# Performance work log

Measured on AMD Instinct MI355X. Metric: run time of the kernel, lower is better.

The kernel has to match this reference:

```python
import jax, jax.numpy as jnp
import numpy as np

B, S, D = 8, 2048, 64
H = 128


def setup_inputs() -> dict:
    key = jax.random.key(0)
    k = jax.random.split(key, 5)
    X = jax.random.normal(k[0], (B, S, D), dtype=jnp.float32)
    Wi = jax.random.normal(k[1], (H, D), dtype=jnp.float32)          # init_layer weight, std=1
    bi = jax.random.normal(k[2], (H,), dtype=jnp.float32)            # init_layer bias, std=1
    Wa = jax.random.normal(k[3], (H * H, D + 1), dtype=jnp.float32) / jnp.sqrt(H)  # vf_A, std=1/sqrt(H)
    Wb = jax.random.normal(k[4], (H, D + 1), dtype=jnp.float32)      # vf_B, std=1
    return {"X": X, "Wi": Wi, "bi": bi, "Wa": Wa, "Wb": Wb}


def reference(X, Wi, bi, Wa, Wb):
    b, s, d = X.shape
    dt = 1.0 / (s - 1)
    # inp: time channel (constant dt) concatenated with scaled input -> [b, s, d+1]
    inp = jnp.concatenate([jnp.full((b, s, 1), dt, dtype=X.dtype), X * dt], axis=-1)
    y0 = X[:, 0] @ Wi.T + bi                       # [b, H]
    Bs = jnp.einsum('bsk,hk->bsh', inp[:, 1:], Wb)  # [b, s-1, H]

    def step(y, xs):
        inp_t, b_t = xs                            # [b, d+1], [b, H]
        A = (inp_t @ Wa.T).reshape(b, H, H)        # per-step transition matrix
        y_new = y + jnp.einsum('bij,bj->bi', A, y) + b_t
        return y_new, y_new

    xs = (jnp.swapaxes(inp[:, 1:], 0, 1), jnp.swapaxes(Bs, 0, 1))  # time-major
    _, ys_rest = jax.lax.scan(step, y0, xs)        # [s-1, b, H]
    ys = jnp.concatenate([y0[:, None, :], jnp.swapaxes(ys_rest, 0, 1)], axis=1)
    return ys
```

## Files before the change

### kernel.cpp

```cpp
#include <hip/hip_runtime.h>
#include <hip/hip_fp16.h>
#include <hip/hip_cooperative_groups.h>

namespace cg = cooperative_groups;


typedef _Float16 h8 __attribute__((ext_vector_type(8)));
typedef float v4f __attribute__((ext_vector_type(4)));
typedef unsigned int uint;

constexpr int B_ = 8, S_ = 2048, D_ = 64, H_ = 128;
constexpr int T_ = S_ - 1;
constexpr int KD = D_ + 1;
constexpr float DTC = 1.0f / 2047.0f;
constexpr int L_ = 8;
constexpr int LSH = 3;
constexpr int NC = 256;

__global__ __launch_bounds__(256) void k_prep(const float* __restrict__ Wa,
                                              _Float16* __restrict__ Wa16B,
                                              float* __restrict__ Wa0,
                                              const float* __restrict__ X,
                                              _Float16* __restrict__ Xs16,
                                              const float* __restrict__ Wb,
                                              float* __restrict__ Bs,
                                              const float* __restrict__ Wi,
                                              const float* __restrict__ bi,
                                              float* __restrict__ out,
                                              float* __restrict__ yb) {
  __shared__ float wb_s[H_ * KD];
  __shared__ float xs[16][D_ + 4];
  int bx = blockIdx.x, tid = threadIdx.x;
  if (bx < 4096) {
    int idx = bx * 256 + tid;
    int r = idx >> 6, kk = idx & 63;
    int rt = r >> 4, n = r & 15;
    int kb = kk >> 5, q = (kk >> 3) & 3, jj = kk & 7;
    float v = Wa[(size_t)r * KD + 1 + kk];
    Wa16B[((((size_t)rt * 2 + kb) * 4 + q) * 16 + n) * 8 + jj] = (_Float16)v;
    if (kk == 0) Wa0[r] = Wa[(size_t)r * KD];
  } else if (bx < 8190) {
    int idx = (bx - 4096) * 256 + tid;
    if (idx < B_ * T_ * 64) {
      int bt = idx >> 6, d = idx & 63;
      int b = bt / T_, s = bt - b * T_;
      Xs16[(size_t)bt * 64 + d] = (_Float16)(X[((size_t)b * S_ + s + 1) * D_ + d] * DTC);
    }
  } else if (bx < 9214) {
    int bt0 = (bx - 8190) * 16;
    for (int i2 = tid; i2 < H_ * KD; i2 += 256) wb_s[i2] = Wb[i2];
    for (int i2 = tid; i2 < 16 * D_; i2 += 256) {
      int sl = i2 >> 6, d = i2 & 63;
      int btg = bt0 + sl;
      float v = 0.f;
      if (btg < B_ * T_) {
        int b = btg / T_, s = btg - b * T_;
        v = X[((size_t)b * S_ + s + 1) * D_ + d] * DTC;
      }
      xs[sl][d] = v;
    }
    __syncthreads();
    int h = tid & 127, sh = tid >> 7;
    const float* wrow = &wb_s[h * KD];
    for (int u = 0; u < 8; u++) {
      int sl = sh * 8 + u;
      int btg = bt0 + sl;
      if (btg >= B_ * T_) break;
      float acc = wrow[0] * DTC;
#pragma unroll 8
      for (int d = 0; d < D_; d++) acc += xs[sl][d] * wrow[1 + d];
      Bs[(size_t)btg * H_ + h] = acc;
    }
  } else {
    int b = bx - 9214;
    if (tid < D_) xs[0][tid] = X[(size_t)b * S_ * D_ + tid];
    __syncthreads();
    if (tid < H_) {
      float acc = bi[tid];
      const float* wr = Wi + tid * D_;
#pragma unroll 8
      for (int d = 0; d < D_; d++) acc += xs[0][d] * wr[d];
      out[(size_t)b * S_ * H_ + tid] = acc;
      yb[(size_t)(b * NC + 0) * H_ + tid] = acc;
    }
  }
}

__global__ __launch_bounds__(256) void k_amat(const _Float16* __restrict__ Xs16,
                                              const _Float16* __restrict__ Wa16B,
                                              const float* __restrict__ Wa0,
                                              _Float16* __restrict__ A_sl,
                                              int c0, int scShift) {
  __shared__ _Float16 sb[32 * 528];
  int tid = threadIdx.x;
  int w = tid >> 6, lane = tid & 63;
  int n = lane & 15, q = lane >> 4;
  int rowbase = blockIdx.x * 32;
  int SCm = ((1 << scShift) << LSH) - 1;

  h8 af[2][2];
#pragma unroll
  for (int mi = 0; mi < 2; mi++) {
    int sidx = rowbase + mi * 16 + n;
    int b = sidx >> (scShift + LSH);
    int rem = sidx & SCm;
    int cc = rem >> LSH, l = rem & (L_ - 1);
    int s = (c0 + cc) * L_ + l;
    if (s >= T_) s = T_ - 1;
    size_t btg = (size_t)b * T_ + s;
#pragma unroll
    for (int kb = 0; kb < 2; kb++)
      af[mi][kb] = *(const h8*)(Xs16 + btg * 64 + kb * 32 + q * 8);
  }

  v4f acc[2][8];
#pragma unroll
  for (int nj = 0; nj < 8; nj++) {
    int ct_g = blockIdx.y * 32 + w * 8 + nj;
    float binit = DTC * Wa0[ct_g * 16 + n];
    h8 bf0 = *(const h8*)(Wa16B + ((((size_t)ct_g * 2 + 0) * 4 + q) * 16 + n) * 8);
    h8 bf1 = *(const h8*)(Wa16B + ((((size_t)ct_g * 2 + 1) * 4 + q) * 16 + n) * 8);
#pragma unroll
    for (int mi = 0; mi < 2; mi++) {
      v4f a;
      a[0] = binit; a[1] = binit; a[2] = binit; a[3] = binit;
      a = __builtin_amdgcn_mfma_f32_16x16x32_f16(af[mi][0], bf0, a, 0, 0, 0);
      a = __builtin_amdgcn_mfma_f32_16x16x32_f16(af[mi][1], bf1, a, 0, 0, 0);
      acc[mi][nj] = a;
    }
  }
#pragma unroll
  for (int mi = 0; mi < 2; mi++)
#pragma unroll
    for (int nj = 0; nj < 8; nj++)
#pragma unroll
      for (int reg = 0; reg < 4; reg++)
        sb[(mi * 16 + q * 4 + reg) * 528 + w * 128 + ((nj * 16 + n) ^ (q * 16))] =
            (_Float16)acc[mi][nj][reg];
  __syncthreads();
#pragma unroll
  for (int it = 0; it < 8; it++) {
    int idx = tid + it * 256;
    int t = idx >> 6, u4 = idx & 63;
    int qt = (t >> 2) & 3;
    uint4 val = *(const uint4*)&sb[t * 528 + ((u4 * 8) ^ (qt * 16))];
    *(uint4*)(A_sl + (size_t)(rowbase + t) * 16384 + blockIdx.y * 512 + u4 * 8) = val;
  }
}

__device__ __forceinline__ void chunkmap_body(const _Float16* __restrict__ A_sl,
                                              const float* __restrict__ Bs,
                                              _Float16* __restrict__ Mr,
                                              float* __restrict__ vch,
                                              int c0, int scShift, int chunk, int tid,
                                              _Float16* Dt, float* v32) {
  int w = tid >> 6, lane = tid & 63;
  int n = lane & 15, q = lane >> 4;
  int SC = 1 << scShift;
  int b = chunk >> scShift;
  int cc = chunk & (SC - 1);
  int c = c0 + cc;
  int sbase = c * L_;
  int nsteps = min(L_, T_ - sbase);
  const _Float16* Abase = A_sl + (size_t)chunk * L_ * 16384;
  size_t btb = (size_t)b * T_ + sbase;

#pragma unroll
  for (int it = 0; it < 8; it++) {
    int idx = tid + it * 256;
    int rowl = idx & 127, c8 = (idx >> 7) * 8;
    uint4 pk = *(const uint4*)(Abase + rowl * 128 + c8);
    const _Float16* hp = (const _Float16*)&pk;
#pragma unroll
    for (int cx = 0; cx < 8; cx++) Dt[(c8 + cx) * 136 + rowl] = hp[cx];
  }
  if (tid < 128) v32[tid] = Bs[btb * 128 + tid];
  h8 idE, idO;
#pragma unroll
  for (int jj = 0; jj < 8; jj++) {
    idE[jj] = (_Float16)((q * 8 + jj == n) ? 1.f : 0.f);
    idO[jj] = (_Float16)((q * 8 + jj == 16 + n) ? 1.f : 0.f);
  }
  __syncthreads();

  v4f acc[2][8];
#pragma unroll
  for (int mi = 0; mi < 2; mi++) {
    int row0 = (2 * w + mi) * 16 + q * 4;
#pragma unroll
    for (int nj = 0; nj < 8; nj++) {
      int col = nj * 16 + n;
      union { uint2 u; _Float16 h[4]; } m2;
      m2.u = *(const uint2*)&Dt[col * 136 + row0];
#pragma unroll
      for (int reg = 0; reg < 4; reg++) acc[mi][nj][reg] = (float)m2.h[reg];
    }
  }

  int r0 = 2 * w * 16 + n, r1 = r0 + 16;
  h8 afA[2][4], afB[2][4];

#define LOADA(dst, l)                                                                \
  {                                                                                  \
    const _Float16* Ag = Abase + (size_t)(l) * 16384;                                \
    _Pragma("unroll")                                                                \
    for (int mi = 0; mi < 2; mi++)                                                   \
      _Pragma("unroll")                                                              \
      for (int kb = 0; kb < 4; kb++)                                                 \
        dst[mi][kb] = *(const h8*)(Ag + ((2 * w + mi) * 16 + n) * 128 + kb * 32 + q * 8); \
  }

#define STEPQ(af, l)                                                                 \
  {                                                                                  \
    _Pragma("unroll")                                                                \
    for (int nj = 0; nj < 8; nj++) {                                                 \
      h8 bfr[4];                                                                     \
      _Pragma("unroll")                                                              \
      for (int kb = 0; kb < 4; kb++)                                                 \
        bfr[kb] = *(const h8*)&Dt[(nj * 16 + n) * 136 + kb * 32 + q * 8];            \
      _Pragma("unroll")                                                              \
      for (int mi = 0; mi < 2; mi++) {                                               \
        _Pragma("unroll")                                                            \
        for (int kb = 0; kb < 4; kb++)                                               \
          acc[mi][nj] = __builtin_amdgcn_mfma_f32_16x16x32_f16(af[mi][kb], bfr[kb], acc[mi][nj], 0, 0, 0); \
        acc[mi][nj] = __builtin_amdgcn_mfma_f32_16x16x32_f16(                        \
            af[mi][nj >> 1], (nj & 1) ? idO : idE, acc[mi][nj], 0, 0, 0);            \
      }                                                                              \
    }                                                                                \
    float dv0 = 0.f, dv1 = 0.f;                                                      \
    _Pragma("unroll")                                                                \
    for (int kb = 0; kb < 4; kb++) {                                                 \
      float4 p0 = *(const float4*)&v32[kb * 32 + q * 8];                             \
      float4 p1 = *(const float4*)&v32[kb * 32 + q * 8 + 4];                         \
      float vk[8] = {p0.x, p0.y, p0.z, p0.w, p1.x, p1.y, p1.z, p1.w};                \
      _Pragma("unroll")                                                              \
      for (int jj = 0; jj < 8; jj++) {                                               \
        dv0 += (float)af[0][kb][jj] * vk[jj];                                        \
        dv1 += (float)af[1][kb][jj] * vk[jj];                                        \
      }                                                                              \
    }                                                                                \
    dv0 += __shfl_xor(dv0, 16); dv0 += __shfl_xor(dv0, 32);                          \
    dv1 += __shfl_xor(dv1, 16); dv1 += __shfl_xor(dv1, 32);                          \
    float vold0 = v32[r0], vold1 = v32[r1];                                          \
    float bs0 = 0.f, bs1 = 0.f;                                                      \
    if (q == 0) {                                                                    \
      bs0 = Bs[(btb + (l)) * 128 + r0];                                              \
      bs1 = Bs[(btb + (l)) * 128 + r1];                                              \
    }                                                                                \
    __syncthreads();                                                                 \
    _Pragma("unroll")                                                                \
    for (int mi = 0; mi < 2; mi++) {                                                 \
      int row0 = (2 * w + mi) * 16 + q * 4;                                          \
      _Pragma("unroll")                                                              \
      for (int nj = 0; nj < 8; nj++) {                                               \
        int col = nj * 16 + n;                                                       \
        union { _Float16 h[4]; uint2 u; } pk;                                        \
        _Pragma("unroll")                                                            \
        for (int reg = 0; reg < 4; reg++) pk.h[reg] = (_Float16)acc[mi][nj][reg];    \
        *(uint2*)&Dt[col * 136 + row0] = pk.u;                                       \
      }                                                                              \
    }                                                                                \
    if (q == 0) {                                                                    \
      v32[r0] = vold0 + dv0 + bs0;                                                   \
      v32[r1] = vold1 + dv1 + bs1;                                                   \
    }                                                                                \
    __syncthreads();                                                                 \
  }

  LOADA(afA, 1);
  for (int l = 1; l < nsteps; l += 2) {
    if (l + 1 < nsteps) LOADA(afB, l + 1);
    STEPQ(afA, l);
    if (l + 2 < nsteps) LOADA(afA, l + 2);
    if (l + 1 < nsteps) STEPQ(afB, l + 1);
  }
#undef LOADA
#undef STEPQ

#pragma unroll
  for (int mi = 0; mi < 2; mi++) {
    int row0 = (2 * w + mi) * 16 + q * 4;
#pragma unroll
    for (int nj = 0; nj < 8; nj++) {
      int col = nj * 16 + n;
#pragma unroll
      for (int reg = 0; reg < 4; reg++)
        Dt[(row0 + reg) * 136 + col] = (_Float16)acc[mi][nj][reg];
    }
  }
  __syncthreads();
  _Float16* og = Mr + (size_t)chunk * 16384;
#pragma unroll
  for (int it = 0; it < 8; it++) {
    int idx = tid + it * 256;
    int rowl = idx >> 4, ch = idx & 15;
    uint4 val = *(const uint4*)&Dt[rowl * 136 + ch * 8];
    *(uint4*)(og + rowl * 128 + ch * 8) = val;
  }
  if (tid < 128) vch[(size_t)chunk * 128 + tid] = v32[tid];
}

__device__ __forceinline__ void comp4_body(const _Float16* __restrict__ in_map,
                                           const float* __restrict__ in_v,
                                           _Float16* __restrict__ out_map,
                                           float* __restrict__ out_v,
                                           int outIdx, int tid,
                                           _Float16* Dt, float* v32) {
  int w = tid >> 6, lane = tid & 63;
  int n = lane & 15, q = lane >> 4;
  size_t nbase = (size_t)outIdx * 4;

  const _Float16* P0 = in_map + nbase * 16384;
#pragma unroll
  for (int it = 0; it < 8; it++) {
    int idx = tid + it * 256;
    int rowl = idx & 127, c8 = (idx >> 7) * 8;
    uint4 pk = *(const uint4*)(P0 + rowl * 128 + c8);
    const _Float16* hp = (const _Float16*)&pk;
#pragma unroll
    for (int cx = 0; cx < 8; cx++) Dt[(c8 + cx) * 136 + rowl] = hp[cx];
  }
  if (tid < 128) v32[tid] = in_v[nbase * 128 + tid];
  h8 idE, idO;
#pragma unroll
  for (int jj = 0; jj < 8; jj++) {
    idE[jj] = (_Float16)((q * 8 + jj == n) ? 1.f : 0.f);
    idO[jj] = (_Float16)((q * 8 + jj == 16 + n) ? 1.f : 0.f);
  }
  __syncthreads();

  v4f acc[2][8];
#pragma unroll
  for (int mi = 0; mi < 2; mi++) {
    int row0 = (2 * w + mi) * 16 + q * 4;
#pragma unroll
    for (int nj = 0; nj < 8; nj++) {
      int col = nj * 16 + n;
      union { uint2 u; _Float16 h[4]; } m2;
      m2.u = *(const uint2*)&Dt[col * 136 + row0];
#pragma unroll
      for (int reg = 0; reg < 4; reg++) acc[mi][nj][reg] = (float)m2.h[reg];
    }
  }

  int r0 = 2 * w * 16 + n, r1 = r0 + 16;
  for (int j = 1; j < 4; j++) {
    const _Float16* Pj = in_map + (nbase + j) * 16384;
    h8 af[2][4];
#pragma unroll
    for (int mi = 0; mi < 2; mi++)
#pragma unroll
      for (int kb = 0; kb < 4; kb++)
        af[mi][kb] = *(const h8*)(Pj + ((2 * w + mi) * 16 + n) * 128 + kb * 32 + q * 8);
#pragma unroll
    for (int nj = 0; nj < 8; nj++) {
      h8 bfr[4];
#pragma unroll
      for (int kb = 0; kb < 4; kb++)
        bfr[kb] = *(const h8*)&Dt[(nj * 16 + n) * 136 + kb * 32 + q * 8];
#pragma unroll
      for (int mi = 0; mi < 2; mi++) {
#pragma unroll
        for (int kb = 0; kb < 4; kb++)
          acc[mi][nj] = __builtin_amdgcn_mfma_f32_16x16x32_f16(af[mi][kb], bfr[kb], acc[mi][nj], 0, 0, 0);
        acc[mi][nj] = __builtin_amdgcn_mfma_f32_16x16x32_f16(
            af[mi][nj >> 1], (nj & 1) ? idO : idE, acc[mi][nj], 0, 0, 0);
      }
    }
    float dv0 = 0.f, dv1 = 0.f;
#pragma unroll
    for (int kb = 0; kb < 4; kb++) {
      float4 p0 = *(const float4*)&v32[kb * 32 + q * 8];
      float4 p1 = *(const float4*)&v32[kb * 32 + q * 8 + 4];
      float vk[8] = {p0.x, p0.y, p0.z, p0.w, p1.x, p1.y, p1.z, p1.w};
#pragma unroll
      for (int jj = 0; jj < 8; jj++) {
        dv0 += (float)af[0][kb][jj] * vk[jj];
        dv1 += (float)af[1][kb][jj] * vk[jj];
      }
    }
    dv0 += __shfl_xor(dv0, 16); dv0 += __shfl_xor(dv0, 32);
    dv1 += __shfl_xor(dv1, 16); dv1 += __shfl_xor(dv1, 32);
    float vold0 = v32[r0], vold1 = v32[r1];
    float vj0 = 0.f, vj1 = 0.f;
    if (q == 0) {
      vj0 = in_v[(nbase + j) * 128 + r0];
      vj1 = in_v[(nbase + j) * 128 + r1];
    }
    __syncthreads();
#pragma unroll
    for (int mi = 0; mi < 2; mi++) {
      int row0 = (2 * w + mi) * 16 + q * 4;
#pragma unroll
      for (int nj = 0; nj < 8; nj++) {
        int col = nj * 16 + n;
        union { _Float16 h[4]; uint2 u; } pk;
#pragma unroll
        for (int reg = 0; reg < 4; reg++) pk.h[reg] = (_Float16)acc[mi][nj][reg];
        *(uint2*)&Dt[col * 136 + row0] = pk.u;
      }
    }
    if (q == 0) {
      v32[r0] = vold0 + dv0 + vj0;
      v32[r1] = vold1 + dv1 + vj1;
    }
    __syncthreads();
  }
#pragma unroll
  for (int mi = 0; mi < 2; mi++) {
    int row0 = (2 * w + mi) * 16 + q * 4;
#pragma unroll
    for (int nj = 0; nj < 8; nj++) {
      int col = nj * 16 + n;
#pragma unroll
      for (int reg = 0; reg < 4; reg++)
        Dt[(row0 + reg) * 136 + col] = (_Float16)acc[mi][nj][reg];
    }
  }
  __syncthreads();
  _Float16* og = out_map + (size_t)outIdx * 16384;
#pragma unroll
  for (int it = 0; it < 8; it++) {
    int idx = tid + it * 256;
    int rowl = idx >> 4, ch = idx & 15;
    uint4 val = *(const uint4*)&Dt[rowl * 136 + ch * 8];
    *(uint4*)(og + rowl * 128 + ch * 8) = val;
  }
  if (tid < 128) out_v[(size_t)outIdx * 128 + tid] = v32[tid];
}

__device__ __forceinline__ void chainsuper_body(const _Float16* __restrict__ Sr,
                                                const float* __restrict__ sv,
                                                float* __restrict__ yb,
                                                int c0, int scShift, int b, int tid,
                                                float* ybuf, float* red) {
  int NS = 1 << (scShift - 2);
  int i = tid >> 1, hh = tid & 1;
  if (tid < 128) ybuf[tid] = yb[(size_t)(b * NC + c0) * 128 + tid];
  __syncthreads();

  uint4 arA[8], arB[8];
  float svA, svB;

#define LOADS(ar, svv, s)                                                            \
  {                                                                                  \
    const uint4* p = (const uint4*)(Sr + (size_t)(b * NS + (s)) * 16384 + i * 128 + hh * 64); \
    _Pragma("unroll")                                                                \
    for (int u = 0; u < 8; u++) ar[u] = p[u];                                        \
    svv = sv[(size_t)(b * NS + (s)) * 128 + i];                                      \
  }

#define STEPS(ar, svv, s)                                                            \
  {                                                                                  \
    float pt = 0.f;                                                                  \
    _Pragma("unroll")                                                                \
    for (int u = 0; u < 8; u++) {                                                    \
      union { uint4 v; _Float16 h[8]; } wv; wv.v = ar[u];                            \
      _Pragma("unroll")                                                              \
      for (int k = 0; k < 8; k++) pt += (float)wv.h[k] * ybuf[hh * 64 + u * 8 + k];  \
    }                                                                                \
    if (hh) red[i] = pt;                                                             \
    __syncthreads();                                                                 \
    if (!hh) {                                                                       \
      float yn = ybuf[i] + pt + red[i] + svv;                                        \
      int cg = c0 + 4 * ((s) + 1);                                                   \
      if (cg < NC) yb[(size_t)(b * NC + cg) * 128 + i] = yn;                         \
      ybuf[i] = yn;                                                                  \
    }                                                                                \
    __syncthreads();                                                                 \
  }

  LOADS(arA, svA, 0);
  int s = 0;
  for (; s + 1 < NS; s += 2) {
    LOADS(arB, svB, s + 1);
    STEPS(arA, svA, s);
    if (s + 2 < NS) LOADS(arA, svA, s + 2);
    STEPS(arB, svB, s + 1);
  }
  if (s < NS) STEPS(arA, svA, s);
#undef LOADS
#undef STEPS
}

__device__ __forceinline__ void emit_body(const _Float16* __restrict__ A_sl,
                                          const float* __restrict__ Bs,
                                          const _Float16* __restrict__ Mr,
                                          const float* __restrict__ vch,
                                          const float* __restrict__ yb,
                                          float* __restrict__ out,
                                          int tid, int b, int c, int kpre, int cbase,
                                          int nst, size_t node0, size_t sidx0, size_t btb,
                                          uint4* arA, float bsA, uint4* arP, float vvP,
                                          float* ybuf, float* red) {
  int i = tid >> 1, hh = tid & 1;
  if (tid < 128) ybuf[tid] = yb[(size_t)(b * NC + cbase) * 128 + tid];
  __syncthreads();

  for (int j = 0; j < kpre; j++) {
    uint4 ar[8];
    float vv;
    if (j == 0) {
#pragma unroll
      for (int u = 0; u < 8; u++) ar[u] = arP[u];
      vv = vvP;
    } else {
      const uint4* p = (const uint4*)(Mr + (node0 + j) * 16384 + i * 128 + hh * 64);
#pragma unroll
      for (int u = 0; u < 8; u++) ar[u] = p[u];
      vv = vch[(node0 + j) * 128 + i];
    }
    float pt = 0.f;
#pragma unroll
    for (int u = 0; u < 8; u++) {
      union { uint4 v; _Float16 h[8]; } wv; wv.v = ar[u];
#pragma unroll
      for (int k = 0; k < 8; k++) pt += (float)wv.h[k] * ybuf[hh * 64 + u * 8 + k];
    }
    if (hh) red[i] = pt;
    __syncthreads();
    if (!hh) {
      float yn = ybuf[i] + pt + red[i] + vv;
      ybuf[i] = yn;
    }
    __syncthreads();
  }

  uint4 arB[8];
  float bsB;

#define LOADR(ar, bsv, l)                                                            \
  {                                                                                  \
    const uint4* p = (const uint4*)(A_sl + (sidx0 + (l)) * 16384 + i * 128 + hh * 64); \
    _Pragma("unroll")                                                                \
    for (int u = 0; u < 8; u++) ar[u] = p[u];                                        \
    bsv = Bs[(btb + (l)) * 128 + i];                                                 \
  }

#define STEPE(ar, bsv, l)                                                            \
  {                                                                                  \
    float pt = 0.f;                                                                  \
    _Pragma("unroll")                                                                \
    for (int u = 0; u < 8; u++) {                                                    \
      union { uint4 v; _Float16 h[8]; } wv; wv.v = ar[u];                            \
      _Pragma("unroll")                                                              \
      for (int k = 0; k < 8; k++) pt += (float)wv.h[k] * ybuf[hh * 64 + u * 8 + k];  \
    }                                                                                \
    if (hh) red[i] = pt;                                                             \
    __syncthreads();                                                                 \
    if (!hh) {                                                                       \
      float yn = ybuf[i] + pt + red[i] + bsv;                                        \
      out[((size_t)b * S_ + (size_t)(c * L_ + (l) + 1)) * 128 + i] = yn;             \
      ybuf[i] = yn;                                                                  \
    }                                                                                \
    __syncthreads();                                                                 \
  }

  for (int l = 0; l < nst; l += 2) {
    if (l + 1 < nst) LOADR(arB, bsB, l + 1);
    STEPE(arA, bsA, l);
    if (l + 2 < nst) LOADR(arA, bsA, l + 2);
    if (l + 1 < nst) STEPE(arB, bsB, l + 1);
  }
#undef LOADR
#undef STEPE
}

__global__ __launch_bounds__(256) void k_chunkmap(const _Float16* __restrict__ A_sl,
                                                  const float* __restrict__ Bs,
                                                  _Float16* __restrict__ Mr,
                                                  float* __restrict__ vch,
                                                  int c0, int scShift) {
  __shared__ _Float16 Dt[128 * 136];
  __shared__ float v32[128];
  chunkmap_body(A_sl, Bs, Mr, vch, c0, scShift, blockIdx.x, threadIdx.x, Dt, v32);
}

__global__ __launch_bounds__(256) void k_comp4(const _Float16* __restrict__ in_map,
                                               const float* __restrict__ in_v,
                                               _Float16* __restrict__ out_map,
                                               float* __restrict__ out_v) {
  __shared__ _Float16 Dt[128 * 136];
  __shared__ float v32[128];
  comp4_body(in_map, in_v, out_map, out_v, blockIdx.x, threadIdx.x, Dt, v32);
}

__global__ __launch_bounds__(256) void k_chainsuper(const _Float16* __restrict__ Sr,
                                                    const float* __restrict__ sv,
                                                    float* __restrict__ yb,
                                                    int c0, int scShift) {
  __shared__ float ybuf[128];
  __shared__ float red[128];
  chainsuper_body(Sr, sv, yb, c0, scShift, blockIdx.x, threadIdx.x, ybuf, red);
}

__global__ __launch_bounds__(256) void k_emit(const _Float16* __restrict__ A_sl,
                                              const float* __restrict__ Bs,
                                              const _Float16* __restrict__ Mr,
                                              const float* __restrict__ vch,
                                              const float* __restrict__ yb,
                                              float* __restrict__ out,
                                              int c0, int scShift) {
  __shared__ float ybuf[128];
  __shared__ float red[128];
  int tid = threadIdx.x;
  int SC = 1 << scShift;
  int b = blockIdx.x >> scShift;
  int cc = blockIdx.x & (SC - 1);
  int c = c0 + cc;
  int i = tid >> 1, hh = tid & 1;
  int kpre = cc & 3;
  int cbase = c - kpre;
  size_t node0 = ((size_t)b << scShift) + (cc & ~3);
  int nst = min(L_, T_ - c * L_);
  size_t sidx0 = (size_t)blockIdx.x * L_;
  size_t btb = (size_t)b * T_ + c * L_;
  uint4 arA[8], arP[8];
  float bsA, vvP = 0.f;
  {
    const uint4* p = (const uint4*)(A_sl + sidx0 * 16384 + i * 128 + hh * 64);
#pragma unroll
    for (int u = 0; u < 8; u++) arA[u] = p[u];
    bsA = Bs[btb * 128 + i];
  }
  if (kpre > 0) {
    const uint4* p2 = (const uint4*)(Mr + node0 * 16384 + i * 128 + hh * 64);
#pragma unroll
    for (int u = 0; u < 8; u++) arP[u] = p2[u];
    vvP = vch[node0 * 128 + i];
  }
  emit_body(A_sl, Bs, Mr, vch, yb, out, tid, b, c, kpre, cbase, nst, node0, sidx0, btb,
            arA, bsA, arP, vvP, ybuf, red);
}

__global__ __launch_bounds__(256, 2) void k_slice(const _Float16* __restrict__ A_sl,
                                                  const float* __restrict__ Bs,
                                                  _Float16* __restrict__ Mr,
                                                  float* __restrict__ vch,
                                                  _Float16* __restrict__ Sr,
                                                  float* __restrict__ sv,
                                                  float* __restrict__ yb,
                                                  float* __restrict__ out,
                                                  int c0, int scShift) {
  __shared__ _Float16 Dt[128 * 136];
  __shared__ float v32[128];
  __shared__ float ybuf[128];
  __shared__ float red[128];
  int tid = threadIdx.x;
  cg::grid_group grid = cg::this_grid();

  chunkmap_body(A_sl, Bs, Mr, vch, c0, scShift, blockIdx.x, tid, Dt, v32);
  grid.sync();

  if (blockIdx.x < (int)(gridDim.x >> 2))
    comp4_body(Mr, vch, Sr, sv, blockIdx.x, tid, Dt, v32);
  grid.sync();

  int SC = 1 << scShift;
  int eb = blockIdx.x >> scShift;
  int ecc = blockIdx.x & (SC - 1);
  int ec = c0 + ecc;
  int i = tid >> 1, hh = tid & 1;
  int kpre = ecc & 3;
  int cbase = ec - kpre;
  size_t node0 = ((size_t)eb << scShift) + (ecc & ~3);
  int nst = min(L_, T_ - ec * L_);
  size_t sidx0 = (size_t)blockIdx.x * L_;
  size_t btb = (size_t)eb * T_ + ec * L_;
  uint4 arA[8], arP[8];
  float bsA, vvP = 0.f;
  {
    const uint4* p = (const uint4*)(A_sl + sidx0 * 16384 + i * 128 + hh * 64);
#pragma unroll
    for (int u = 0; u < 8; u++) arA[u] = p[u];
    bsA = Bs[btb * 128 + i];
  }
  if (kpre > 0) {
    const uint4* p2 = (const uint4*)(Mr + node0 * 16384 + i * 128 + hh * 64);
#pragma unroll
    for (int u = 0; u < 8; u++) arP[u] = p2[u];
    vvP = vch[node0 * 128 + i];
  }

  if (blockIdx.x < B_)
    chainsuper_body(Sr, sv, yb, c0, scShift, blockIdx.x, tid, ybuf, red);
  grid.sync();

  emit_body(A_sl, Bs, Mr, vch, yb, out, tid, eb, ec, kpre, cbase, nst, node0, sidx0, btb,
            arA, bsA, arP, vvP, ybuf, red);
}

__global__ __launch_bounds__(256) void k_seq(const float* __restrict__ X,
                                             const float* __restrict__ Wa,
                                             const float* __restrict__ Wb,
                                             float* __restrict__ out) {
  int b = blockIdx.x, tid = threadIdx.x;
  int i = tid >> 1, hh = tid & 1;
  __shared__ float y[H_], red[H_], xs[D_], bts[H_];
  if (tid < H_) y[tid] = out[(size_t)b * S_ * H_ + tid];
  __syncthreads();
  for (int t = 1; t < S_; t++) {
    if (tid < D_) xs[tid] = X[((size_t)b * S_ + t) * D_ + tid] * DTC;
    __syncthreads();
    if (tid < H_) {
      const float* wr = Wb + tid * KD;
      float acc = wr[0] * DTC;
#pragma unroll 8
      for (int d = 0; d < D_; d++) acc += xs[d] * wr[1 + d];
      bts[tid] = acc;
    }
    float part = 0.f;
    const float* yhalf = &y[hh * 64];
    for (int j = 0; j < 64; j++) {
      const float* wr = Wa + ((size_t)(i * H_) + hh * 64 + j) * KD;
      float a = wr[0] * DTC;
#pragma unroll 8
      for (int d = 0; d < D_; d++) a += xs[d] * wr[1 + d];
      part += a * yhalf[j];
    }
    if (hh) red[i] = part;
    __syncthreads();
    if (!hh) {
      float yn = y[i] + part + red[i] + bts[i];
      out[((size_t)b * S_ + t) * H_ + i] = yn;
      y[i] = yn;
    }
    __syncthreads();
  }
}

__global__ __launch_bounds__(128) void k_y0f(const float* __restrict__ X,
                                             const float* __restrict__ Wi,
                                             const float* __restrict__ bi,
                                             float* __restrict__ out) {
  int b = blockIdx.x, h = threadIdx.x;
  __shared__ float xs[D_];
  if (h < D_) xs[h] = X[(size_t)b * S_ * D_ + h];
  __syncthreads();
  float acc = bi[h];
  const float* wr = Wi + h * D_;
#pragma unroll 8
  for (int d = 0; d < D_; d++) acc += xs[d] * wr[d];
  out[(size_t)b * S_ * H_ + h] = acc;
}

extern "C" void kernel_launch(void* const* d_in, const int* in_sizes, int n_in,
                              void* d_out, int out_size, void* d_ws, size_t ws_size,
                              hipStream_t stream) {
  (void)in_sizes; (void)n_in; (void)out_size;
  const float* X  = (const float*)d_in[0];
  const float* Wi = (const float*)d_in[1];
  const float* bi = (const float*)d_in[2];
  const float* Wa = (const float*)d_in[3];
  const float* Wb = (const float*)d_in[4];
  float* out = (float*)d_out;
  char* ws = (char*)d_ws;

  size_t off = 0;
  auto alloc = [&](size_t bytes) { size_t o = off; off = (off + bytes + 255) & ~(size_t)255; return o; };
  size_t oBs  = alloc((size_t)B_ * T_ * 128 * 4);
  size_t oYb  = alloc((size_t)B_ * NC * 128 * 4);
  size_t oWaB = alloc((size_t)64 * 16384 * 2);
  size_t oWa0 = alloc((size_t)16384 * 4);
  size_t oXs  = alloc((size_t)B_ * T_ * 64 * 2);
  size_t fixed = off;

  const size_t APC  = (size_t)B_ * L_ * 16384 * 2;
  const size_t MRPC = (size_t)B_ * 16384 * 2;
  const size_t VCPC = (size_t)B_ * 128 * 4;
  const size_t SRPC = (size_t)B_ * 16384 * 2 / 4;
  const size_t SVPC = (size_t)B_ * 128;
  const size_t PER_SC = APC + MRPC + VCPC + SRPC + SVPC + 5 * 256;

  int SC = 0;
  if (ws_size > fixed) {
    size_t avail = ws_size - fixed;
    SC = 64;
    while (SC >= 4 && (size_t)SC * PER_SC > avail) SC >>= 1;
    if (SC < 4) SC = 0;
  }
  if (SC < 4) {
    k_y0f<<<B_, 128, 0, stream>>>(X, Wi, bi, out);
    k_seq<<<B_, 256, 0, stream>>>(X, Wa, Wb, out);
    return;
  }
  int scShift = __builtin_ctz(SC);

  size_t oMr = alloc((size_t)SC * MRPC);
  size_t oVc = alloc((size_t)SC * VCPC);
  size_t oSr = alloc((size_t)SC * SRPC);
  size_t oSv = alloc((size_t)SC * SVPC);
  size_t oA  = alloc((size_t)SC * APC);

  float*    Bs    = (float*)(ws + oBs);
  float*    yb    = (float*)(ws + oYb);
  _Float16* Wa16B = (_Float16*)(ws + oWaB);
  float*    Wa0   = (float*)(ws + oWa0);
  _Float16* Xs16  = (_Float16*)(ws + oXs);
  _Float16* Mr    = (_Float16*)(ws + oMr);
  float*    vch   = (float*)(ws + oVc);
  _Float16* Sr    = (_Float16*)(ws + oSr);
  float*    sv    = (float*)(ws + oSv);
  _Float16* A_sl  = (_Float16*)(ws + oA);

  k_prep<<<9222, 256, 0, stream>>>(Wa, Wa16B, Wa0, X, Xs16, Wb, Bs, Wi, bi, out, yb);

  static int coopNB = -1;
  if (coopNB < 0) {
    int nb = 0;
    coopNB = (hipOccupancyMaxActiveBlocksPerMultiprocessor(&nb, k_slice, 256, 0) == hipSuccess)
                 ? nb : 0;
  }

  int nslices = NC / SC;
  int chunks = B_ * SC;
  int amat_gx = (B_ * SC * L_) / 32;
  bool useCoop = ((size_t)coopNB * 256 >= (size_t)chunks);
  for (int si = 0; si < nslices; si++) {
    int c0 = si * SC;
    k_amat<<<dim3(amat_gx, 32), 256, 0, stream>>>(Xs16, Wa16B, Wa0, A_sl, c0, scShift);
    bool done = false;
    if (useCoop) {
      const _Float16* aA = A_sl; const float* aB = Bs;
      _Float16* aM = Mr; float* aV = vch;
      _Float16* aS = Sr; float* aSv = sv;
      float* aY = yb; float* aO = out;
      int ac0 = c0, asc = scShift;
      void* args[] = {&aA, &aB, &aM, &aV, &aS, &aSv, &aY, &aO, &ac0, &asc};
      if (hipLaunchCooperativeKernel((const void*)k_slice, dim3(chunks), dim3(256),
                                     args, 0, stream) == hipSuccess)
        done = true;
      else
        useCoop = false;
    }
    if (!done) {
      k_chunkmap<<<chunks, 256, 0, stream>>>(A_sl, Bs, Mr, vch, c0, scShift);
      k_comp4<<<chunks / 4, 256, 0, stream>>>(Mr, vch, Sr, sv);
      k_chainsuper<<<B_, 256, 0, stream>>>(Sr, sv, yb, c0, scShift);
      k_emit<<<chunks, 256, 0, stream>>>(A_sl, Bs, Mr, vch, yb, out, c0, scShift);
    }
  }
}
```

Baseline: 671.4 us.

## Replace cooperative grid-sync slice kernel with last-block-done atomic chaining

Removes the cooperative k_slice kernel and its grid-wide barriers. Chunk-map, 4-way composition and per-batch chain steps now run in one kernel, k_cmc, where the last arriving block of each group (tracked by atomic counters) does the next stage. Emit is launched as a separate kernel. This avoids grid.sync stalls and the cooperative launch path. The cost is an extra launch per slice, serialized tail work on a few blocks, and counter state that must be reset between uses.

After: 843.9 us. +25.7%, slower.

```diff
diff --git a/kernel.cpp b/kernel.cpp
--- a/kernel.cpp
+++ b/kernel.cpp
@@ -1,8 +1,5 @@
 #include <hip/hip_runtime.h>
 #include <hip/hip_fp16.h>
-#include <hip/hip_cooperative_groups.h>
-
-namespace cg = cooperative_groups;
 
 
 typedef _Float16 h8 __attribute__((ext_vector_type(8)));
@@ -27,7 +24,8 @@
                                               const float* __restrict__ Wi,
                                               const float* __restrict__ bi,
                                               float* __restrict__ out,
-                                              float* __restrict__ yb) {
+                                              float* __restrict__ yb,
+                                              int* __restrict__ cnt) {
   __shared__ float wb_s[H_ * KD];
   __shared__ float xs[16][D_ + 4];
   int bx = blockIdx.x, tid = threadIdx.x;
@@ -74,6 +72,9 @@
   } else {
     int b = bx - 9214;
     if (tid < D_) xs[0][tid] = X[(size_t)b * S_ * D_ + tid];
+    if (b == 0 && tid >= 128) {
+      for (int j = tid - 128; j < 136; j += 128) cnt[j] = 0;
+    }
     __syncthreads();
     if (tid < H_) {
       float acc = bi[tid];
@@ -483,6 +484,52 @@
 #undef STEPS
 }
 
+__global__ __launch_bounds__(256) void k_cmc(const _Float16* __restrict__ A_sl,
+                                             const float* __restrict__ Bs,
+                                             _Float16* __restrict__ Mr,
+                                             float* __restrict__ vch,
+                                             _Float16* __restrict__ Sr,
+                                             float* __restrict__ sv,
+                                             float* __restrict__ yb,
+                                             int* __restrict__ gcnt,
+                                             int* __restrict__ bcnt,
+                                             int c0, int scShift) {
+  __shared__ _Float16 Dt[128 * 136];
+  __shared__ float v32[128];
+  __shared__ float ybuf[128];
+  __shared__ float red[128];
+  __shared__ int flag;
+  int tid = threadIdx.x;
+
+  chunkmap_body(A_sl, Bs, Mr, vch, c0, scShift, blockIdx.x, tid, Dt, v32);
+  __syncthreads();
+  int g = blockIdx.x >> 2;
+  if (tid == 0) {
+    int old = __hip_atomic_fetch_add(&gcnt[g], 1, __ATOMIC_ACQ_REL,
+                                     __HIP_MEMORY_SCOPE_AGENT);
+    flag = (old == 3) ? 1 : 0;
+  }
+  __syncthreads();
+  if (!flag) return;
+
+  comp4_body(Mr, vch, Sr, sv, g, tid, Dt, v32);
+  __syncthreads();
+  int NSm1 = (1 << (scShift - 2)) - 1;
+  int bb = g >> (scShift - 2);
+  if (tid == 0) {
+    __hip_atomic_store(&gcnt[g], 0, __ATOMIC_RELAXED, __HIP_MEMORY_SCOPE_AGENT);
+    int old2 = __hip_atomic_fetch_add(&bcnt[bb], 1, __ATOMIC_ACQ_REL,
+                                      __HIP_MEMORY_SCOPE_AGENT);
+    flag = (old2 == NSm1) ? 1 : 0;
+  }
+  __syncthreads();
+  if (!flag) return;
+
+  chainsuper_body(Sr, sv, yb, c0, scShift, bb, tid, ybuf, red);
+  if (tid == 0)
+    __hip_atomic_store(&bcnt[bb], 0, __ATOMIC_RELAXED, __HIP_MEMORY_SCOPE_AGENT);
+}
+
 __device__ __forceinline__ void emit_body(const _Float16* __restrict__ A_sl,
                                           const float* __restrict__ Bs,
                                           const _Float16* __restrict__ Mr,
@@ -564,34 +611,6 @@
   }
 #undef LOADR
 #undef STEPE
-}
-
-__global__ __launch_bounds__(256) void k_chunkmap(const _Float16* __restrict__ A_sl,
-                                                  const float* __restrict__ Bs,
-                                                  _Float16* __restrict__ Mr,
-                                                  float* __restrict__ vch,
-                                                  int c0, int scShift) {
-  __shared__ _Float16 Dt[128 * 136];
-  __shared__ float v32[128];
-  chunkmap_body(A_sl, Bs, Mr, vch, c0, scShift, blockIdx.x, threadIdx.x, Dt, v32);
-}
-
-__global__ __launch_bounds__(256) void k_comp4(const _Float16* __restrict__ in_map,
-                                               const float* __restrict__ in_v,
-                                               _Float16* __restrict__ out_map,
-                                               float* __restrict__ out_v) {
-  __shared__ _Float16 Dt[128 * 136];
-  __shared__ float v32[128];
-  comp4_body(in_map, in_v, out_map, out_v, blockIdx.x, threadIdx.x, Dt, v32);
-}
-
-__global__ __launch_bounds__(256) void k_chainsuper(const _Float16* __restrict__ Sr,
-                                                    const float* __restrict__ sv,
-                                                    float* __restrict__ yb,
-                                                    int c0, int scShift) {
-  __shared__ float ybuf[128];
-  __shared__ float red[128];
-  chainsuper_body(Sr, sv, yb, c0, scShift, blockIdx.x, threadIdx.x, ybuf, red);
 }
 
 __global__ __launch_bounds__(256) void k_emit(const _Float16* __restrict__ A_sl,
@@ -633,63 +652,6 @@
             arA, bsA, arP, vvP, ybuf, red);
 }
 
-__global__ __launch_bounds__(256, 2) void k_slice(const _Float16* __restrict__ A_sl,
-                                                  const float* __restrict__ Bs,
-                                                  _Float16* __restrict__ Mr,
-                                                  float* __restrict__ vch,
-                                                  _Float16* __restrict__ Sr,
-                                                  float* __restrict__ sv,
-                                                  float* __restrict__ yb,
-                                                  float* __restrict__ out,
-                                                  int c0, int scShift) {
-  __shared__ _Float16 Dt[128 * 136];
-  __shared__ float v32[128];
-  __shared__ float ybuf[128];
-  __shared__ float red[128];
-  int tid = threadIdx.x;
-  cg::grid_group grid = cg::this_grid();
-
-  chunkmap_body(A_sl, Bs, Mr, vch, c0, scShift, blockIdx.x, tid, Dt, v32);
-  grid.sync();
-
-  if (blockIdx.x < (int)(gridDim.x >> 2))
-    comp4_body(Mr, vch, Sr, sv, blockIdx.x, tid, Dt, v32);
-  grid.sync();
-
-  int SC = 1 << scShift;
-  int eb = blockIdx.x >> scShift;
-  int ecc = blockIdx.x & (SC - 1);
-  int ec = c0 + ecc;
-  int i = tid >> 1, hh = tid & 1;
-  int kpre = ecc & 3;
-  int cbase = ec - kpre;
-  size_t node0 = ((size_t)eb << scShift) + (ecc & ~3);
-  int nst = min(L_, T_ - ec * L_);
-  size_t sidx0 = (size_t)blockIdx.x * L_;
-  size_t btb = (size_t)eb * T_ + ec * L_;
-  uint4 arA[8], arP[8];
-  float bsA, vvP = 0.f;
-  {
-    const uint4* p = (const uint4*)(A_sl + sidx0 * 16384 + i * 128 + hh * 64);
-#pragma unroll
-    for (int u = 0; u < 8; u++) arA[u] = p[u];
-    bsA = Bs[btb * 128 + i];
-  }
-  if (kpre > 0) {
-    const uint4* p2 = (const uint4*)(Mr + node0 * 16384 + i * 128 + hh * 64);
-#pragma unroll
-    for (int u = 0; u < 8; u++) arP[u] = p2[u];
-    vvP = vch[node0 * 128 + i];
-  }
-
-  if (blockIdx.x < B_)
-    chainsuper_body(Sr, sv, yb, c0, scShift, blockIdx.x, tid, ybuf, red);
-  grid.sync();
-
-  emit_body(A_sl, Bs, Mr, vch, yb, out, tid, eb, ec, kpre, cbase, nst, node0, sidx0, btb,
-            arA, bsA, arP, vvP, ybuf, red);
-}
-
 __global__ __launch_bounds__(256) void k_seq(const float* __restrict__ X,
                                              const float* __restrict__ Wa,
                                              const float* __restrict__ Wb,
@@ -763,6 +725,7 @@
   size_t oWaB = alloc((size_t)64 * 16384 * 2);
   size_t oWa0 = alloc((size_t)16384 * 4);
   size_t oXs  = alloc((size_t)B_ * T_ * 64 * 2);
+  size_t oCnt = alloc(1024);
   size_t fixed = off;
 
   const size_t APC  = (size_t)B_ * L_ * 16384 * 2;
@@ -797,47 +760,23 @@
   _Float16* Wa16B = (_Float16*)(ws + oWaB);
   float*    Wa0   = (float*)(ws + oWa0);
   _Float16* Xs16  = (_Float16*)(ws + oXs);
+  int*      gcnt  = (int*)(ws + oCnt);
+  int*      bcnt  = gcnt + 128;
   _Float16* Mr    = (_Float16*)(ws + oMr);
   float*    vch   = (float*)(ws + oVc);
   _Float16* Sr    = (_Float16*)(ws + oSr);
   float*    sv    = (float*)(ws + oSv);
   _Float16* A_sl  = (_Float16*)(ws + oA);
 
-  k_prep<<<9222, 256, 0, stream>>>(Wa, Wa16B, Wa0, X, Xs16, Wb, Bs, Wi, bi, out, yb);
-
-  static int coopNB = -1;
-  if (coopNB < 0) {
-    int nb = 0;
-    coopNB = (hipOccupancyMaxActiveBlocksPerMultiprocessor(&nb, k_slice, 256, 0) == hipSuccess)
-                 ? nb : 0;
-  }
+  k_prep<<<9222, 256, 0, stream>>>(Wa, Wa16B, Wa0, X, Xs16, Wb, Bs, Wi, bi, out, yb, gcnt);
 
   int nslices = NC / SC;
   int chunks = B_ * SC;
   int amat_gx = (B_ * SC * L_) / 32;
-  bool useCoop = ((size_t)coopNB * 256 >= (size_t)chunks);
   for (int si = 0; si < nslices; si++) {
     int c0 = si * SC;
     k_amat<<<dim3(amat_gx, 32), 256, 0, stream>>>(Xs16, Wa16B, Wa0, A_sl, c0, scShift);
-    bool done = false;
-    if (useCoop) {
-      const _Float16* aA = A_sl; const float* aB = Bs;
-      _Float16* aM = Mr; float* aV = vch;
-      _Float16* aS = Sr; float* aSv = sv;
-      float* aY = yb; float* aO = out;
-      int ac0 = c0, asc = scShift;
-      void* args[] = {&aA, &aB, &aM, &aV, &aS, &aSv, &aY, &aO, &ac0, &asc};
-      if (hipLaunchCooperativeKernel((const void*)k_slice, dim3(chunks), dim3(256),
-                                     args, 0, stream) == hipSuccess)
-        done = true;
-      else
-        useCoop = false;
-    }
-    if (!done) {
-      k_chunkmap<<<chunks, 256, 0, stream>>>(A_sl, Bs, Mr, vch, c0, scShift);
-      k_comp4<<<chunks / 4, 256, 0, stream>>>(Mr, vch, Sr, sv);
-      k_chainsuper<<<B_, 256, 0, stream>>>(Sr, sv, yb, c0, scShift);
-      k_emit<<<chunks, 256, 0, stream>>>(A_sl, Bs, Mr, vch, yb, out, c0, scShift);
-    }
-  }
-}
+    k_cmc<<<chunks, 256, 0, stream>>>(A_sl, Bs, Mr, vch, Sr, sv, yb, gcnt, bcnt, c0, scShift);
+    k_emit<<<chunks, 256, 0, stream>>>(A_sl, Bs, Mr, vch, yb, out, c0, scShift);
+  }
+}
```
